# Kernel tuning notes

Measured on AMD Instinct MI355X. Metric: run time of the kernel, lower is better.

## Reference

```python
import jax, jax.numpy as jnp
import numpy as np

B = 65536   # batch
D = 48      # despawn feature dim (level*4)
T = 768     # transformer feature dim
F = 512     # fusion_dim
L = 64      # latent_dim
K = 2048    # num_embeddings
H = 4       # attention heads
COMMIT = 0.25


def _ln(x, w, b):
    m = x.mean(-1, keepdims=True)
    v = ((x - m) ** 2).mean(-1, keepdims=True)
    return (x - m) * jax.lax.rsqrt(v + 1e-5) * w + b


def _mha(q, k, v, in_w, in_b, out_w, out_b):
    # torch nn.MultiheadAttention (batch_first), q/k/v: [B, S, F]
    f = q.shape[-1]; dh = f // H
    wq, wk, wv = in_w[:f], in_w[f:2 * f], in_w[2 * f:]
    bq, bk, bv = in_b[:f], in_b[f:2 * f], in_b[2 * f:]
    def proj(x, w, bb):
        y = x @ w.T + bb
        return y.reshape(x.shape[0], x.shape[1], H, dh)
    qh, kh, vh = proj(q, wq, bq), proj(k, wk, bk), proj(v, wv, bv)
    s = jnp.einsum('bqhd,bkhd->bhqk', qh, kh) / jnp.sqrt(jnp.float32(dh))
    a = jax.nn.softmax(s, axis=-1)
    o = jnp.einsum('bhqk,bkhd->bqhd', a, vh).reshape(q.shape[0], q.shape[1], f)
    return o @ out_w.T + out_b


def setup_inputs() -> dict:
    key = jax.random.key(0)
    ks = jax.random.split(key, 32)
    rn = lambda k, s, sc=0.02: jax.random.normal(k, s, jnp.float32) * sc
    return {
        'df': jax.random.normal(ks[0], (B, D), jnp.float32),
        'tf': jax.random.normal(ks[1], (B, T), jnp.float32),
        # HierarchicalFusion params
        'dp_w': rn(ks[2], (F, D)), 'dp_b': jnp.zeros((F,), jnp.float32),
        'tp_w': rn(ks[3], (F, T)), 'tp_b': jnp.zeros((F,), jnp.float32),
        'in_w': rn(ks[4], (3 * F, F)), 'in_b': jnp.zeros((3 * F,), jnp.float32),
        'out_w': rn(ks[5], (F, F)), 'out_b': jnp.zeros((F,), jnp.float32),
        'n1_w': jnp.ones((F,), jnp.float32), 'n1_b': jnp.zeros((F,), jnp.float32),
        'n2_w': jnp.ones((F,), jnp.float32), 'n2_b': jnp.zeros((F,), jnp.float32),
        # encoder: Linear(2F,F) -> LN -> ReLU -> Linear(F,L)
        'e_w1': rn(ks[6], (F, 2 * F)), 'e_b1': jnp.zeros((F,), jnp.float32),
        'e_lnw': jnp.ones((F,), jnp.float32), 'e_lnb': jnp.zeros((F,), jnp.float32),
        'e_w2': rn(ks[7], (L, F)), 'e_b2': jnp.zeros((L,), jnp.float32),
        # VQ codebook, uniform(-1/K, 1/K) as in the module
        'codebook': jax.random.uniform(ks[8], (K, L), jnp.float32, -1.0 / K, 1.0 / K),
        # decoder: Linear(L,F) -> ReLU -> Linear(F,2F)
        'd_w1': rn(ks[9], (F, L)), 'd_b1': jnp.zeros((F,), jnp.float32),
        'd_w2': rn(ks[10], (2 * F, F)), 'd_b2': jnp.zeros((2 * F,), jnp.float32),
    }


def reference(df, tf, dp_w, dp_b, tp_w, tp_b, in_w, in_b, out_w, out_b,
              n1_w, n1_b, n2_w, n2_b, e_w1, e_b1, e_lnw, e_lnb, e_w2, e_b2,
              codebook, d_w1, d_b1, d_w2, d_b2):
    # HierarchicalFusion: project to [B,1,F] tokens, cross-attend both ways
    d = (df @ dp_w.T + dp_b)[:, None, :]
    t = (tf @ tp_w.T + tp_b)[:, None, :]
    d2 = d + _mha(_ln(d, n1_w, n1_b), _ln(t, n1_w, n1_b), _ln(t, n1_w, n1_b),
                  in_w, in_b, out_w, out_b)
    t2 = t + _mha(_ln(t, n2_w, n2_b), _ln(d, n2_w, n2_b), _ln(d, n2_w, n2_b),
                  in_w, in_b, out_w, out_b)
    fused = jnp.concatenate([d2, t2], axis=1).reshape(d2.shape[0], 2 * F)  # [B, 2F]
    # encoder
    h = jax.nn.relu(_ln(fused @ e_w1.T + e_b1, e_lnw, e_lnb)) @ e_w2.T + e_b2  # [B, L]
    # vector quantization: cdist^2 + argmin + gather (equiv to one-hot @ emb)
    dist = (h ** 2).sum(1, keepdims=True) + (codebook ** 2).sum(1) - 2.0 * h @ codebook.T
    idx = jnp.argmin(dist, axis=1)                 # [B]
    quant = codebook[idx]                          # [B, L]
    loss = jnp.mean((jax.lax.stop_gradient(quant) - h) ** 2) + \
           COMMIT * jnp.mean((quant - jax.lax.stop_gradient(h)) ** 2)
    z_q = h + jax.lax.stop_gradient(quant - h)     # straight-through
    # decoder
    rec = jax.nn.relu(z_q @ d_w1.T + d_b1) @ d_w2.T + d_b2  # [B, 2F]
    return rec, loss, idx
```

## Files before the change

kernel.cpp:

```cpp
#include <hip/hip_runtime.h>
#include <math.h>

typedef long long ll;
typedef double f64x4 __attribute__((ext_vector_type(4)));

#define BN 65536LL
#define LOSS_OFF (BN * 1024LL)
#define IDX_OFF  (LOSS_OFF + 1LL)

#define WF_W1 0LL
#define WF_RT (WF_W1 + BN * 512LL)
#define WF_CN (WF_RT + 2048LL * 1024LL)
#define WF_LP (WF_CN + 2048LL)

#define BSTR 522

template<int MODE>
__global__ __launch_bounds__(512, 4)
void k_mmf(const float* __restrict__ A0, const float* __restrict__ A1, int K,
           const float* __restrict__ W, const float* __restrict__ bias,
           const float* __restrict__ resid,
           const float* __restrict__ lnw, const float* __restrict__ lnb,
           float* __restrict__ Y, float* __restrict__ Y2)
{
  __shared__ double As64[2][16][33];
  __shared__ double poolB[2][4176];
  __shared__ float msh[32], rsh[32];
  double (*red)[128] = (double(*)[128])poolB[0];

  const int tid = threadIdx.x;
  const int w = tid >> 6, l = tid & 63;
  const int q16 = l >> 4, l15 = l & 15;
  const int cbase = w * 64;
  const ll r0 = (ll)blockIdx.x * 32;
  const int strideA0 = A1 ? 512 : K;
  const int arow = tid >> 4, ak = tid & 15;

  f64x4 acc[8];
#pragma unroll
  for (int f = 0; f < 8; ++f) acc[f] = (f64x4){0.0, 0.0, 0.0, 0.0};

  {
    float av = A0[(r0 + arow) * (ll)strideA0 + ak];
    float4 bv4[4];
#pragma unroll
    for (int m = 0; m < 4; ++m) {
      const int s = m * 512 + tid;
      const int col = s >> 2, kq = s & 3;
      bv4[m] = *(const float4*)(W + (ll)col * K + kq * 4);
    }
    As64[0][ak][arow] = (double)av;
    float* B0 = (float*)poolB[0];
#pragma unroll
    for (int m = 0; m < 4; ++m) {
      const int s = m * 512 + tid;
      const int col = s >> 2, kq = s & 3;
      B0[(kq*4+0)*BSTR + col] = bv4[m].x;
      B0[(kq*4+1)*BSTR + col] = bv4[m].y;
      B0[(kq*4+2)*BSTR + col] = bv4[m].z;
      B0[(kq*4+3)*BSTR + col] = bv4[m].w;
    }
  }
  __syncthreads();

  int cur = 0;
  for (int kc = 0; kc < K; kc += 16) {
    const bool more = (kc + 16) < K;
    float av; float4 bv4[4];
    if (more) {
      const int cidx = kc + 16 + ak;
      if (A1 && cidx >= 512) av = A1[(r0 + arow) * 512LL + (cidx - 512)];
      else                   av = A0[(r0 + arow) * (ll)strideA0 + cidx];
#pragma unroll
      for (int m = 0; m < 4; ++m) {
        const int s = m * 512 + tid;
        const int col = s >> 2, kq = s & 3;
        bv4[m] = *(const float4*)(W + (ll)col * K + kc + 16 + kq * 4);
      }
    }
    {
      const double (*A_)[33] = As64[cur];
      const float* B_ = (const float*)poolB[cur];
#pragma unroll
      for (int kq = 0; kq < 4; ++kq) {
        const int kk = kq * 4 + q16;
        const double a0 = A_[kk][l15];
        const double a1 = A_[kk][16 + l15];
#pragma unroll
        for (int nt = 0; nt < 4; ++nt) {
          const double b = (double)B_[kk * BSTR + cbase + nt*16 + l15];
          acc[nt]     = __builtin_amdgcn_mfma_f64_16x16x4f64(a0, b, acc[nt],     0, 0, 0);
          acc[4 + nt] = __builtin_amdgcn_mfma_f64_16x16x4f64(a1, b, acc[4 + nt], 0, 0, 0);
        }
      }
    }
    if (more) {
      As64[cur ^ 1][ak][arow] = (double)av;
      float* Bn = (float*)poolB[cur ^ 1];
#pragma unroll
      for (int m = 0; m < 4; ++m) {
        const int s = m * 512 + tid;
        const int col = s >> 2, kq = s & 3;
        Bn[(kq*4+0)*BSTR + col] = bv4[m].x;
        Bn[(kq*4+1)*BSTR + col] = bv4[m].y;
        Bn[(kq*4+2)*BSTR + col] = bv4[m].z;
        Bn[(kq*4+3)*BSTR + col] = bv4[m].w;
      }
    }
    __syncthreads();
    cur ^= 1;
  }

  float o[8][4];
#pragma unroll
  for (int mt = 0; mt < 2; ++mt)
#pragma unroll
    for (int nt = 0; nt < 4; ++nt)
#pragma unroll
      for (int bb = 0; bb < 4; ++bb) {
        const int row = mt*16 + q16*4 + bb;
        const int col = cbase + nt*16 + l15;
        const float mm = (float)acc[mt*4+nt][bb];
        const float y1 = mm + bias[col];
        o[mt*4+nt][bb] = resid ? (resid[(r0 + row) * 512LL + col] + y1) : y1;
      }

  if (MODE != 2) {
#pragma unroll
    for (int mt = 0; mt < 2; ++mt)
#pragma unroll
      for (int nt = 0; nt < 4; ++nt)
#pragma unroll
        for (int bb = 0; bb < 4; ++bb) {
          const int row = mt*16 + q16*4 + bb;
          const int col = cbase + nt*16 + l15;
          Y[(r0 + row) * 512LL + col] = o[mt*4+nt][bb];
        }
  }
  if (MODE == 0) return;

#pragma unroll
  for (int mt = 0; mt < 2; ++mt)
#pragma unroll
    for (int bb = 0; bb < 4; ++bb) {
      const int row = mt*16 + q16*4 + bb;
      double s = 0.0;
#pragma unroll
      for (int nt = 0; nt < 4; ++nt) s += (double)o[mt*4+nt][bb];
      red[row][w*16 + l15] = s;
    }
  __syncthreads();
  if (tid < 32) {
    double s = 0.0;
    for (int x = 0; x < 128; ++x) s += red[tid][x];
    msh[tid] = (float)(s * (1.0 / 512.0));
  }
  __syncthreads();
#pragma unroll
  for (int mt = 0; mt < 2; ++mt)
#pragma unroll
    for (int bb = 0; bb < 4; ++bb) {
      const int row = mt*16 + q16*4 + bb;
      const float m32 = msh[row];
      double s2 = 0.0;
#pragma unroll
      for (int nt = 0; nt < 4; ++nt) {
        o[mt*4+nt][bb] = o[mt*4+nt][bb] - m32;
        const float sq = o[mt*4+nt][bb] * o[mt*4+nt][bb];
        s2 += (double)sq;
      }
      red[row][w*16 + l15] = s2;
    }
  __syncthreads();
  if (tid < 32) {
    double s = 0.0;
    for (int x = 0; x < 128; ++x) s += red[tid][x];
    const float v32 = (float)(s * (1.0 / 512.0));
    const float a32 = v32 + 1e-5f;
    const float sq32 = (float)sqrt((double)a32);
    rsh[tid] = (float)(1.0 / (double)sq32);
  }
  __syncthreads();
  {
    float* dst = (MODE == 1) ? Y2 : Y;
#pragma unroll
    for (int mt = 0; mt < 2; ++mt)
#pragma unroll
      for (int bb = 0; bb < 4; ++bb) {
        const int row = mt*16 + q16*4 + bb;
        const float rs = rsh[row];
#pragma unroll
        for (int nt = 0; nt < 4; ++nt) {
          const int col = cbase + nt*16 + l15;
          float v = ((o[mt*4+nt][bb] * rs) * lnw[col]) + lnb[col];
          if (MODE == 2) v = fmaxf(v, 0.f);
          dst[(r0 + row) * 512LL + col] = v;
        }
      }
  }
}

__global__ __launch_bounds__(256)
void k_ln(const float* __restrict__ X, const float* __restrict__ w,
          const float* __restrict__ b, float* __restrict__ Y, int relu)
{
  const int tid = threadIdx.x;
  const int lane = tid & 63, wid = tid >> 6;
  const ll row = (ll)blockIdx.x * 4 + wid;
  const ll base = row * 512;

  float xv[8];
#pragma unroll
  for (int j = 0; j < 8; ++j) xv[j] = X[base + j*64 + lane];

  double s = 0.0;
#pragma unroll
  for (int j = 0; j < 8; ++j) s += (double)xv[j];
#pragma unroll
  for (int off = 32; off > 0; off >>= 1) s += __shfl_down(s, off, 64);
  s = __shfl(s, 0, 64);
  const float m32 = (float)(s * (1.0 / 512.0));

  float xm[8];
  double s2 = 0.0;
#pragma unroll
  for (int j = 0; j < 8; ++j) {
    xm[j] = xv[j] - m32;
    const float sq = xm[j] * xm[j];
    s2 += (double)sq;
  }
#pragma unroll
  for (int off = 32; off > 0; off >>= 1) s2 += __shfl_down(s2, off, 64);
  s2 = __shfl(s2, 0, 64);
  const float v32 = (float)(s2 * (1.0 / 512.0));
  const float a32 = v32 + 1e-5f;
  const float sq32 = (float)sqrt((double)a32);
  const float rs32 = (float)(1.0 / (double)sq32);

#pragma unroll
  for (int j = 0; j < 8; ++j) {
    float o = ((xm[j] * rs32) * w[j*64 + lane]) + b[j*64 + lane];
    if (relu) o = fmaxf(o, 0.f);
    Y[base + j*64 + lane] = o;
  }
}

__global__ __launch_bounds__(256)
void k_pre(const float* __restrict__ cbk, const float* __restrict__ d_w1,
           const float* __restrict__ d_b1, const float* __restrict__ d_w2,
           const float* __restrict__ d_b2,
           float* __restrict__ rect, float* __restrict__ cnorm)
{
  __shared__ float cbs16[16][68];
  __shared__ float pbuf[16][516];
  const int tid = threadIdx.x;
  const int bb = blockIdx.x;

  if (bb < 128) {
    const int e0 = bb * 16;
    {
      const int e = tid >> 4, q = tid & 15;
      const float4 v = *(const float4*)(cbk + (ll)(e0 + e) * 64 + q * 4);
      *(float4*)&cbs16[e][q*4] = v;
    }
    __syncthreads();
    {
      double pa0[16], pa1[16];
#pragma unroll
      for (int e = 0; e < 16; ++e) { pa0[e] = 0.0; pa1[e] = 0.0; }
      const int i0 = tid * 2;
      for (int l = 0; l < 64; l += 4) {
        const float4 w0 = *(const float4*)(d_w1 + (ll)i0 * 64 + l);
        const float4 w1 = *(const float4*)(d_w1 + (ll)(i0 + 1) * 64 + l);
#pragma unroll
        for (int e = 0; e < 16; ++e) {
          const float4 c4 = *(const float4*)&cbs16[e][l];
          pa0[e] = fma((double)w0.x,(double)c4.x, fma((double)w0.y,(double)c4.y,
                   fma((double)w0.z,(double)c4.z, fma((double)w0.w,(double)c4.w, pa0[e]))));
          pa1[e] = fma((double)w1.x,(double)c4.x, fma((double)w1.y,(double)c4.y,
                   fma((double)w1.z,(double)c4.z, fma((double)w1.w,(double)c4.w, pa1[e]))));
        }
      }
      const double db0 = (double)d_b1[i0], db1 = (double)d_b1[i0 + 1];
#pragma unroll
      for (int e = 0; e < 16; ++e) {
        pbuf[e][i0]     = (float)fmax(pa0[e] + db0, 0.0);
        pbuf[e][i0 + 1] = (float)fmax(pa1[e] + db1, 0.0);
      }
    }
    __syncthreads();
    {
      double ra[16][4];
#pragma unroll
      for (int e = 0; e < 16; ++e)
#pragma unroll
        for (int k = 0; k < 4; ++k) ra[e][k] = 0.0;
      const int o4 = tid * 4;
      for (int i4 = 0; i4 < 512; i4 += 4) {
        const float4 w0 = *(const float4*)(d_w2 + (ll)(o4+0) * 512 + i4);
        const float4 w1 = *(const float4*)(d_w2 + (ll)(o4+1) * 512 + i4);
        const float4 w2 = *(const float4*)(d_w2 + (ll)(o4+2) * 512 + i4);
        const float4 w3 = *(const float4*)(d_w2 + (ll)(o4+3) * 512 + i4);
#pragma unroll
        for (int e = 0; e < 16; ++e) {
          const float4 p4 = *(const float4*)&pbuf[e][i4];
          ra[e][0] = fma((double)w0.x,(double)p4.x, fma((double)w0.y,(double)p4.y,
                     fma((double)w0.z,(double)p4.z, fma((double)w0.w,(double)p4.w, ra[e][0]))));
          ra[e][1] = fma((double)w1.x,(double)p4.x, fma((double)w1.y,(double)p4.y,
                     fma((double)w1.z,(double)p4.z, fma((double)w1.w,(double)p4.w, ra[e][1]))));
          ra[e][2] = fma((double)w2.x,(double)p4.x, fma((double)w2.y,(double)p4.y,
                     fma((double)w2.z,(double)p4.z, fma((double)w2.w,(double)p4.w, ra[e][2]))));
          ra[e][3] = fma((double)w3.x,(double)p4.x, fma((double)w3.y,(double)p4.y,
                     fma((double)w3.z,(double)p4.z, fma((double)w3.w,(double)p4.w, ra[e][3]))));
        }
      }
      const float4 db = *(const float4*)(d_b2 + o4);
#pragma unroll
      for (int e = 0; e < 16; ++e) {
        *(float4*)(rect + (ll)(e0 + e) * 1024 + o4) =
          make_float4((float)(ra[e][0]+(double)db.x), (float)(ra[e][1]+(double)db.y),
                      (float)(ra[e][2]+(double)db.z), (float)(ra[e][3]+(double)db.w));
      }
    }
  } else {
    for (int k = tid; k < 2048; k += 256) {
      double s = 0.0;
      for (int l = 0; l < 64; ++l) {
        const float c = cbk[(ll)k * 64 + l];
        const float q = c * c;
        s += (double)q;
      }
      cnorm[k] = (float)s;
    }
  }
}

__global__ __launch_bounds__(256)
void k_head(const float* __restrict__ rin, const float* __restrict__ e_w2,
            const float* __restrict__ e_b2, const float* __restrict__ cbk,
            const float* __restrict__ cnorm, const float* __restrict__ rect,
            float* __restrict__ dout, double* __restrict__ lossP)
{
  __shared__ float As[32][17];
  __shared__ float Bsh[16][68];
  __shared__ float hbuf[32][68];
  __shared__ float hA[32];
  __shared__ float cbs[128][68];
  __shared__ float cns[128];
  __shared__ float redv[32][33];
  __shared__ int   redi[32][33];
  __shared__ int   idxs[32];
  __shared__ double lred[256];
  const int tid = threadIdx.x;
  const int tx = tid & 31, ty = tid >> 5;
  const ll r0 = (ll)blockIdx.x * 32;

  double acc2[4][2];
#pragma unroll
  for (int i = 0; i < 4; ++i) { acc2[i][0] = 0.0; acc2[i][1] = 0.0; }
  for (int kc = 0; kc < 512; kc += 16) {
    if (tid < 128) {
      const int rr = tid >> 2, q = tid & 3;
      const float4 v = *(const float4*)(rin + (r0 + rr) * 512LL + kc + q * 4);
      As[rr][q*4+0] = v.x; As[rr][q*4+1] = v.y; As[rr][q*4+2] = v.z; As[rr][q*4+3] = v.w;
    }
    {
      const int c = tid >> 2, q = tid & 3;
      const float4 v = *(const float4*)(e_w2 + (ll)c * 512 + kc + q * 4);
      Bsh[q*4+0][c] = v.x; Bsh[q*4+1][c] = v.y; Bsh[q*4+2][c] = v.z; Bsh[q*4+3][c] = v.w;
    }
    __syncthreads();
#pragma unroll
    for (int j = 0; j < 16; ++j) {
      const double b0 = (double)Bsh[j][tx*2+0], b1 = (double)Bsh[j][tx*2+1];
      const double a0 = (double)As[ty*4+0][j], a1 = (double)As[ty*4+1][j];
      const double a2 = (double)As[ty*4+2][j], a3 = (double)As[ty*4+3][j];
      acc2[0][0] = fma(a0,b0,acc2[0][0]); acc2[0][1] = fma(a0,b1,acc2[0][1]);
      acc2[1][0] = fma(a1,b0,acc2[1][0]); acc2[1][1] = fma(a1,b1,acc2[1][1]);
      acc2[2][0] = fma(a2,b0,acc2[2][0]); acc2[2][1] = fma(a2,b1,acc2[2][1]);
      acc2[3][0] = fma(a3,b0,acc2[3][0]); acc2[3][1] = fma(a3,b1,acc2[3][1]);
    }
    __syncthreads();
  }
  {
    const float eb0 = e_b2[tx*2+0], eb1 = e_b2[tx*2+1];
#pragma unroll
    for (int i = 0; i < 4; ++i) {
      hbuf[ty*4+i][tx*2+0] = (float)acc2[i][0] + eb0;
      hbuf[ty*4+i][tx*2+1] = (float)acc2[i][1] + eb1;
    }
  }
  __syncthreads();

  if (tid < 32) {
    double s = 0.0;
    for (int l = 0; l < 64; ++l) {
      const float hh = hbuf[tid][l];
      const float q = hh * hh;
      s += (double)q;
    }
    hA[tid] = (float)s;
  }
  __syncthreads();

  float bestv[4]; int besti[4];
#pragma unroll
  for (int i = 0; i < 4; ++i) { bestv[i] = 3.4e38f; besti[i] = 0; }
  for (int c0 = 0; c0 < 2048; c0 += 128) {
#pragma unroll
    for (int m = 0; m < 8; ++m) {
      const int l = m * 256 + tid;
      const int kk = l >> 4, q = l & 15;
      const float4 v = *(const float4*)(cbk + (ll)(c0 + kk) * 64 + q * 4);
      *(float4*)&cbs[kk][q*4] = v;
    }
    if (tid < 128) cns[tid] = cnorm[c0 + tid];
    __syncthreads();
    double dacc[4][4];
#pragma unroll
    for (int i = 0; i < 4; ++i)
#pragma unroll
      for (int j2 = 0; j2 < 4; ++j2) dacc[i][j2] = 0.0;
#pragma unroll
    for (int l = 0; l < 64; l += 4) {
      float4 ha[4], cv[4];
#pragma unroll
      for (int i = 0; i < 4; ++i) ha[i] = *(const float4*)&hbuf[ty*4+i][l];
#pragma unroll
      for (int j2 = 0; j2 < 4; ++j2) cv[j2] = *(const float4*)&cbs[tx + 32*j2][l];
#pragma unroll
      for (int i = 0; i < 4; ++i)
#pragma unroll
        for (int j2 = 0; j2 < 4; ++j2) {
          dacc[i][j2] = fma((double)ha[i].x, (double)cv[j2].x, dacc[i][j2]);
          dacc[i][j2] = fma((double)ha[i].y, (double)cv[j2].y, dacc[i][j2]);
          dacc[i][j2] = fma((double)ha[i].z, (double)cv[j2].z, dacc[i][j2]);
          dacc[i][j2] = fma((double)ha[i].w, (double)cv[j2].w, dacc[i][j2]);
        }
    }
#pragma unroll
    for (int i = 0; i < 4; ++i)
#pragma unroll
      for (int j2 = 0; j2 < 4; ++j2) {
        const float C32 = (float)dacc[i][j2];
        const float D = 2.0f * C32;
        const float E = hA[ty*4+i] + cns[tx + 32*j2];
        const float dist = E - D;
        const int kg = c0 + tx + 32*j2;
        if (dist < bestv[i]) { bestv[i] = dist; besti[i] = kg; }
      }
    __syncthreads();
  }
#pragma unroll
  for (int i = 0; i < 4; ++i) { redv[ty*4+i][tx] = bestv[i]; redi[ty*4+i][tx] = besti[i]; }
  __syncthreads();
  if (tid < 32) {
    float bv = redv[tid][0]; int bi = redi[tid][0];
    for (int x = 1; x < 32; ++x) {
      const float v = redv[tid][x]; const int ii = redi[tid][x];
      if (v < bv || (v == bv && ii < bi)) { bv = v; bi = ii; }
    }
    idxs[tid] = bi;
    dout[IDX_OFF + r0 + tid] = (float)bi;
  }
  __syncthreads();

  {
    const int r = tid >> 3, sl = tid & 7;
    const float* cq = cbk + (ll)idxs[r] * 64 + sl * 8;
    double s = 0.0;
#pragma unroll
    for (int e = 0; e < 8; ++e) {
      const float dx = cq[e] - hbuf[r][sl*8 + e];
      const float sq = dx * dx;
      s += (double)sq;
    }
    lred[tid] = s;
  }
  __syncthreads();
  for (int off = 128; off > 0; off >>= 1) {
    if (tid < off) lred[tid] += lred[tid + off];
    __syncthreads();
  }
  if (tid == 0) lossP[blockIdx.x] = lred[0];

  for (int m = 0; m < 32; ++m) {
    const float4 v = *(const float4*)(rect + (ll)idxs[m] * 1024 + tid * 4);
    *(float4*)(dout + (r0 + m) * 1024 + tid * 4) = v;
  }
}

__global__ __launch_bounds__(256)
void k_loss(const double* __restrict__ lossP, float* __restrict__ dout)
{
  __shared__ double red[256];
  const int tid = threadIdx.x;
  double s = 0.0;
  for (int i = tid; i < 2048; i += 256) s += lossP[i];
  red[tid] = s;
  __syncthreads();
  for (int off = 128; off > 0; off >>= 1) {
    if (tid < off) red[tid] += red[tid + off];
    __syncthreads();
  }
  if (tid == 0) {
    const float m1 = (float)(red[0] * (1.0 / 4194304.0));
    dout[LOSS_OFF] = m1 + 0.25f * m1;
  }
}

extern "C" void kernel_launch(void* const* d_in, const int* in_sizes, int n_in,
                              void* d_out, int out_size, void* d_ws, size_t ws_size,
                              hipStream_t stream)
{
  (void)in_sizes; (void)n_in; (void)out_size; (void)ws_size;
  const float* df    = (const float*)d_in[0];
  const float* tf    = (const float*)d_in[1];
  const float* dp_w  = (const float*)d_in[2];
  const float* dp_b  = (const float*)d_in[3];
  const float* tp_w  = (const float*)d_in[4];
  const float* tp_b  = (const float*)d_in[5];
  const float* in_w  = (const float*)d_in[6];
  const float* in_b  = (const float*)d_in[7];
  const float* out_w = (const float*)d_in[8];
  const float* out_b = (const float*)d_in[9];
  const float* n1w   = (const float*)d_in[10];
  const float* n1b   = (const float*)d_in[11];
  const float* n2w   = (const float*)d_in[12];
  const float* n2b   = (const float*)d_in[13];
  const float* e_w1  = (const float*)d_in[14];
  const float* e_b1  = (const float*)d_in[15];
  const float* e_lnw = (const float*)d_in[16];
  const float* e_lnb = (const float*)d_in[17];
  const float* e_w2  = (const float*)d_in[18];
  const float* e_b2  = (const float*)d_in[19];
  const float* cbk   = (const float*)d_in[20];
  const float* d_w1  = (const float*)d_in[21];
  const float* d_b1  = (const float*)d_in[22];
  const float* d_w2  = (const float*)d_in[23];
  const float* d_b2  = (const float*)d_in[24];
  float* out = (float*)d_out;
  float* ws  = (float*)d_ws;

  float* S0 = out;
  float* S1 = out + BN * 512LL;
  float* S2 = ws + WF_W1;
  float* RT = ws + WF_RT;
  float* CN = ws + WF_CN;
  double* LP = (double*)(ws + WF_LP);

  const float* wv = in_w + 1024LL * 512LL;
  const float* bv = in_b + 1024LL;

  k_pre<<<129, 256, 0, stream>>>(cbk, d_w1, d_b1, d_w2, d_b2, RT, CN);

  k_mmf<1><<<2048, 512, 0, stream>>>(df, nullptr, 48, dp_w, dp_b, nullptr,
                                     n2w, n2b, S0, S1);
  k_mmf<0><<<2048, 512, 0, stream>>>(S1, nullptr, 512, wv, bv, nullptr,
                                     nullptr, nullptr, S1, nullptr);
  k_mmf<0><<<2048, 512, 0, stream>>>(tf, nullptr, 768, tp_w, tp_b, nullptr,
                                     nullptr, nullptr, S2, nullptr);
  k_mmf<0><<<2048, 512, 0, stream>>>(S1, nullptr, 512, out_w, out_b, S2,
                                     nullptr, nullptr, S1, nullptr);
  k_ln<<<16384, 256, 0, stream>>>(S2, n1w, n1b, S2, 0);
  k_mmf<0><<<2048, 512, 0, stream>>>(S2, nullptr, 512, wv, bv, nullptr,
                                     nullptr, nullptr, S2, nullptr);
  k_mmf<0><<<2048, 512, 0, stream>>>(S2, nullptr, 512, out_w, out_b, S0,
                                     nullptr, nullptr, S2, nullptr);
  k_mmf<2><<<2048, 512, 0, stream>>>(S2, S1, 1024, e_w1, e_b1, nullptr,
                                     e_lnw, e_lnb, S2, nullptr);
  k_head<<<2048, 256, 0, stream>>>(S2, e_w2, e_b2, cbk, CN, RT, out, LP);
  k_loss<<<1, 256, 0, stream>>>(LP, out);
}
```

Baseline: 5.034 ms.

## Fold LayerNorm into next GEMM's A-load using per-row stats

The projection GEMMs now emit only per-row mean and reciprocal std (MODE 3) instead of writing a normalized copy of their output. The following in-projection GEMM applies LayerNorm on the fly while loading its A tile (LNA template flag). This removes the standalone k_ln kernel and the extra normalized output write, cutting global memory traffic and one launch. The cost is a few extra per-element ops and stat/weight loads inside the GEMM's A-load path.

Measured after the change: 5.044 ms, median of 2. About the same (+0.2%).

```diff
diff --git a/kernel.cpp b/kernel.cpp
--- a/kernel.cpp
+++ b/kernel.cpp
@@ -12,16 +12,20 @@
 #define WF_RT (WF_W1 + BN * 512LL)
 #define WF_CN (WF_RT + 2048LL * 1024LL)
 #define WF_LP (WF_CN + 2048LL)
+#define WF_SD (WF_LP + 4096LL)
+#define WF_ST (WF_SD + BN * 2LL)
 
 #define BSTR 522
 
-template<int MODE>
+template<int MODE, int LNA>
 __global__ __launch_bounds__(512, 4)
 void k_mmf(const float* __restrict__ A0, const float* __restrict__ A1, int K,
            const float* __restrict__ W, const float* __restrict__ bias,
            const float* __restrict__ resid,
            const float* __restrict__ lnw, const float* __restrict__ lnb,
-           float* __restrict__ Y, float* __restrict__ Y2)
+           float* __restrict__ Y, float* __restrict__ Y2,
+           const float2* __restrict__ astats,
+           const float* __restrict__ alnw, const float* __restrict__ alnb)
 {
   __shared__ double As64[2][16][33];
   __shared__ double poolB[2][4176];
@@ -42,6 +46,10 @@
 
   {
     float av = A0[(r0 + arow) * (ll)strideA0 + ak];
+    if (LNA) {
+      const float2 st = astats[r0 + arow];
+      av = ((av - st.x) * st.y) * alnw[ak] + alnb[ak];
+    }
     float4 bv4[4];
 #pragma unroll
     for (int m = 0; m < 4; ++m) {
@@ -71,6 +79,10 @@
       const int cidx = kc + 16 + ak;
       if (A1 && cidx >= 512) av = A1[(r0 + arow) * 512LL + (cidx - 512)];
       else                   av = A0[(r0 + arow) * (ll)strideA0 + cidx];
+      if (LNA) {
+        const float2 st = astats[r0 + arow];
+        av = ((av - st.x) * st.y) * alnw[cidx] + alnb[cidx];
+      }
 #pragma unroll
       for (int m = 0; m < 4; ++m) {
         const int s = m * 512 + tid;
@@ -181,8 +193,11 @@
     rsh[tid] = (float)(1.0 / (double)sq32);
   }
   __syncthreads();
+  if (MODE == 3) {
+    if (tid < 32) ((float2*)Y2)[r0 + tid] = make_float2(msh[tid], rsh[tid]);
+    return;
+  }
   {
-    float* dst = (MODE == 1) ? Y2 : Y;
 #pragma unroll
     for (int mt = 0; mt < 2; ++mt)
 #pragma unroll
@@ -194,54 +209,9 @@
           const int col = cbase + nt*16 + l15;
           float v = ((o[mt*4+nt][bb] * rs) * lnw[col]) + lnb[col];
           if (MODE == 2) v = fmaxf(v, 0.f);
-          dst[(r0 + row) * 512LL + col] = v;
+          Y[(r0 + row) * 512LL + col] = v;
         }
       }
-  }
-}
-
-__global__ __launch_bounds__(256)
-void k_ln(const float* __restrict__ X, const float* __restrict__ w,
-          const float* __restrict__ b, float* __restrict__ Y, int relu)
-{
-  const int tid = threadIdx.x;
-  const int lane = tid & 63, wid = tid >> 6;
-  const ll row = (ll)blockIdx.x * 4 + wid;
-  const ll base = row * 512;
-
-  float xv[8];
-#pragma unroll
-  for (int j = 0; j < 8; ++j) xv[j] = X[base + j*64 + lane];
-
-  double s = 0.0;
-#pragma unroll
-  for (int j = 0; j < 8; ++j) s += (double)xv[j];
-#pragma unroll
-  for (int off = 32; off > 0; off >>= 1) s += __shfl_down(s, off, 64);
-  s = __shfl(s, 0, 64);
-  const float m32 = (float)(s * (1.0 / 512.0));
-
-  float xm[8];
-  double s2 = 0.0;
-#pragma unroll
-  for (int j = 0; j < 8; ++j) {
-    xm[j] = xv[j] - m32;
-    const float sq = xm[j] * xm[j];
-    s2 += (double)sq;
-  }
-#pragma unroll
-  for (int off = 32; off > 0; off >>= 1) s2 += __shfl_down(s2, off, 64);
-  s2 = __shfl(s2, 0, 64);
-  const float v32 = (float)(s2 * (1.0 / 512.0));
-  const float a32 = v32 + 1e-5f;
-  const float sq32 = (float)sqrt((double)a32);
-  const float rs32 = (float)(1.0 / (double)sq32);
-
-#pragma unroll
-  for (int j = 0; j < 8; ++j) {
-    float o = ((xm[j] * rs32) * w[j*64 + lane]) + b[j*64 + lane];
-    if (relu) o = fmaxf(o, 0.f);
-    Y[base + j*64 + lane] = o;
   }
 }
 
@@ -548,27 +518,35 @@
   float* RT = ws + WF_RT;
   float* CN = ws + WF_CN;
   double* LP = (double*)(ws + WF_LP);
+  float* SD = ws + WF_SD;
+  float* ST = ws + WF_ST;
 
   const float* wv = in_w + 1024LL * 512LL;
   const float* bv = in_b + 1024LL;
 
   k_pre<<<129, 256, 0, stream>>>(cbk, d_w1, d_b1, d_w2, d_b2, RT, CN);
 
-  k_mmf<1><<<2048, 512, 0, stream>>>(df, nullptr, 48, dp_w, dp_b, nullptr,
-                                     n2w, n2b, S0, S1);
-  k_mmf<0><<<2048, 512, 0, stream>>>(S1, nullptr, 512, wv, bv, nullptr,
-                                     nullptr, nullptr, S1, nullptr);
-  k_mmf<0><<<2048, 512, 0, stream>>>(tf, nullptr, 768, tp_w, tp_b, nullptr,
-                                     nullptr, nullptr, S2, nullptr);
-  k_mmf<0><<<2048, 512, 0, stream>>>(S1, nullptr, 512, out_w, out_b, S2,
-                                     nullptr, nullptr, S1, nullptr);
-  k_ln<<<16384, 256, 0, stream>>>(S2, n1w, n1b, S2, 0);
-  k_mmf<0><<<2048, 512, 0, stream>>>(S2, nullptr, 512, wv, bv, nullptr,
-                                     nullptr, nullptr, S2, nullptr);
-  k_mmf<0><<<2048, 512, 0, stream>>>(S2, nullptr, 512, out_w, out_b, S0,
-                                     nullptr, nullptr, S2, nullptr);
-  k_mmf<2><<<2048, 512, 0, stream>>>(S2, S1, 1024, e_w1, e_b1, nullptr,
-                                     e_lnw, e_lnb, S2, nullptr);
+  k_mmf<3,0><<<2048, 512, 0, stream>>>(df, nullptr, 48, dp_w, dp_b, nullptr,
+                                       nullptr, nullptr, S0, SD,
+                                       nullptr, nullptr, nullptr);
+  k_mmf<0,1><<<2048, 512, 0, stream>>>(S0, nullptr, 512, wv, bv, nullptr,
+                                       nullptr, nullptr, S1, nullptr,
+                                       (const float2*)SD, n2w, n2b);
+  k_mmf<3,0><<<2048, 512, 0, stream>>>(tf, nullptr, 768, tp_w, tp_b, nullptr,
+                                       nullptr, nullptr, S2, ST,
+                                       nullptr, nullptr, nullptr);
+  k_mmf<0,0><<<2048, 512, 0, stream>>>(S1, nullptr, 512, out_w, out_b, S2,
+                                       nullptr, nullptr, S1, nullptr,
+                                       nullptr, nullptr, nullptr);
+  k_mmf<0,1><<<2048, 512, 0, stream>>>(S2, nullptr, 512, wv, bv, nullptr,
+                                       nullptr, nullptr, S2, nullptr,
+                                       (const float2*)ST, n1w, n1b);
+  k_mmf<0,0><<<2048, 512, 0, stream>>>(S2, nullptr, 512, out_w, out_b, S0,
+                                       nullptr, nullptr, S2, nullptr,
+                                       nullptr, nullptr, nullptr);
+  k_mmf<2,0><<<2048, 512, 0, stream>>>(S2, S1, 1024, e_w1, e_b1, nullptr,
+                                       e_lnw, e_lnb, S2, nullptr,
+                                       nullptr, nullptr, nullptr);
   k_head<<<2048, 256, 0, stream>>>(S2, e_w2, e_b2, cbk, CN, RT, out, LP);
   k_loss<<<1, 256, 0, stream>>>(LP, out);
 }
```
